# Kernel tuning notes

Hardware: AMD Instinct MI355X
Metric: run time of the kernel (lower is better)

## Reference

```python
import jax, jax.numpy as jnp
import numpy as np

B, L, H, M, E, NH, R = 4, 512, 1024, 128, 64, 16, 1024   # docs, seq, hidden, mentions, entities, heads, pairs
D, BLK, C = 768, 64, 97                                   # embed_size, block_size, num_class


def setup_inputs() -> dict:
    key = jax.random.key(0)
    ks = jax.random.split(key, 9)
    seq_lhs = jax.random.normal(ks[0], (B, L, H), jnp.float32)
    ent_lhs = jax.random.normal(ks[1], (B, M, H), jnp.float32)
    ent_to_seq_attn = jax.random.uniform(ks[2], (B, NH, M, L), jnp.float32)
    entity_id_labels = jax.random.randint(ks[3], (B, M), 0, E, jnp.int32)
    hts = jax.random.randint(ks[4], (B, R, 2), 0, E, jnp.int32)
    Wh = jax.random.normal(ks[5], (2 * H, D), jnp.float32) * 0.02
    Wt = jax.random.normal(ks[6], (2 * H, D), jnp.float32) * 0.02
    Wb = jax.random.normal(ks[7], (D * BLK, C), jnp.float32) * 0.02
    return dict(seq_lhs=seq_lhs, ent_lhs=ent_lhs, ent_to_seq_attn=ent_to_seq_attn,
                entity_id_labels=entity_id_labels, hts=hts,
                Wh=Wh, bh=jnp.zeros((D,), jnp.float32),
                Wt=Wt, bt=jnp.zeros((D,), jnp.float32),
                Wb=Wb, bb=jnp.zeros((C,), jnp.float32))


def reference(seq_lhs, ent_lhs, ent_to_seq_attn, entity_id_labels, hts, Wh, bh, Wt, bt, Wb, bb):
    # --- hrt_pool: segment logsumexp / mean over mentions per entity ---
    mask = entity_id_labels[:, None, :] == jnp.arange(E, dtype=entity_id_labels.dtype)[None, :, None]  # [B,E,M]
    cnt = mask.sum(-1)  # [B,E]
    neg = jnp.asarray(-1e30, ent_lhs.dtype)
    masked = jnp.where(mask[..., None], ent_lhs[:, None, :, :], neg)          # [B,E,M,H]
    lse = jax.nn.logsumexp(masked, axis=2)                                    # [B,E,H]
    ent_emb = jnp.where((cnt > 0)[..., None], lse, 0.0)
    mf = mask.astype(ent_to_seq_attn.dtype)
    attn_sum = jnp.einsum('bem,bhml->behl', mf, ent_to_seq_attn)              # [B,E,NH,L]
    denom = jnp.maximum(cnt, 1).astype(attn_sum.dtype)[..., None, None]
    ent_attn = jnp.where((cnt > 0)[..., None, None], attn_sum / denom, 0.0)
    # --- gather head/tail entities per pair ---
    h_idx, t_idx = hts[..., 0], hts[..., 1]                                   # [B,R]
    hs = jnp.take_along_axis(ent_emb, h_idx[..., None], axis=1)               # [B,R,H]
    ts = jnp.take_along_axis(ent_emb, t_idx[..., None], axis=1)
    h_attn = jnp.take_along_axis(ent_attn, h_idx[..., None, None], axis=1)    # [B,R,NH,L]
    t_attn = jnp.take_along_axis(ent_attn, t_idx[..., None, None], axis=1)
    ht_attn = (h_attn * t_attn).mean(axis=2)                                  # [B,R,L]
    ht_attn = ht_attn / (ht_attn.sum(-1, keepdims=True) + 1e-5)
    rel = jnp.einsum('brl,bld->brd', ht_attn, seq_lhs)                        # [B,R,H]
    # --- extractors + block bilinear ---
    hcat = jnp.concatenate([hs, rel], -1).reshape(B * R, 2 * H)
    tcat = jnp.concatenate([ts, rel], -1).reshape(B * R, 2 * H)
    hv = jnp.tanh(hcat @ Wh + bh)
    tv = jnp.tanh(tcat @ Wt + bt)
    b1 = hv.reshape(-1, D // BLK, BLK)
    b2 = tv.reshape(-1, D // BLK, BLK)
    bl = (b1[:, :, :, None] * b2[:, :, None, :]).reshape(-1, D * BLK)
    return bl @ Wb + bb                                                       # [B*R, C]
```

## Files before the change

kernel.cpp:

```cpp
#include <hip/hip_runtime.h>
#include <hip/hip_bf16.h>
#include <math.h>

#define B_  4
#define L_  512
#define H_  1024
#define M_  128
#define E_  64
#define NH_ 16
#define R_  1024
#define D_  768
#define BLK_ 64
#define C_  97
#define NROW (B_*R_)
#define KB_  (D_/BLK_)

typedef __attribute__((ext_vector_type(8))) unsigned short ushort8;
typedef __attribute__((ext_vector_type(4))) unsigned short ushort4v;
typedef __attribute__((ext_vector_type(8))) short s8;
typedef __attribute__((ext_vector_type(4))) float f4;

__device__ __forceinline__ unsigned short f2bf(float x) {
    unsigned u = __builtin_bit_cast(unsigned, x);
    unsigned r = (u + 0x7fffu + ((u >> 16) & 1u)) >> 16;
    return (unsigned short)r;
}
__device__ __forceinline__ float bf2f(unsigned short h) {
    unsigned u = ((unsigned)h) << 16;
    return __builtin_bit_cast(float, u);
}
__device__ __forceinline__ float lo16f(unsigned u) { return __builtin_bit_cast(float, u << 16); }
__device__ __forceinline__ float hi16f(unsigned u) { return __builtin_bit_cast(float, u & 0xffff0000u); }

__device__ __forceinline__ void gload_lds16(const unsigned short* g, unsigned short* l)
{
    __builtin_amdgcn_global_load_lds(
        (const __attribute__((address_space(1))) unsigned int*)g,
        (__attribute__((address_space(3))) unsigned int*)l, 16, 0, 0);
}


__global__ __launch_bounds__(256) void fused_prep(
    const float* __restrict__ Wh, const float* __restrict__ Wt,
    unsigned short* __restrict__ WhT, unsigned short* __restrict__ WtT,
    const float* __restrict__ Wb, unsigned short* __restrict__ WbT,
    const float* __restrict__ seq_lhs, unsigned short* __restrict__ seqB,
    const float* __restrict__ ent_lhs, const int* __restrict__ labels,
    unsigned short* __restrict__ ent_embB,
    const float* __restrict__ attn, unsigned short* __restrict__ ent_attnB,
    const float* __restrict__ bb, const float* __restrict__ bh,
    const float* __restrict__ bt,
    float* __restrict__ out, float* __restrict__ Ph, float* __restrict__ Pt)
{
    __shared__ __attribute__((aligned(16))) float smem[6208];
    int bx = blockIdx.x, tid = threadIdx.x;

    if (bx < 3072) {
        int z = bx / 1536, rem = bx % 1536;
        int ky = rem / 24, kx = rem % 24;
        const float* in = z ? Wt : Wh;
        unsigned short* outp = z ? WtT : WhT;
        int n0 = kx*32, k0 = ky*32;
        float (*tile)[33] = (float(*)[33])smem;
        int tx = tid & 31, ty = tid >> 5;
        #pragma unroll
        for (int p = 0; p < 4; ++p)
            tile[ty + p*8][tx] = in[((size_t)(k0 + ty + p*8))*D_ + n0 + tx];
        __syncthreads();
        #pragma unroll
        for (int p = 0; p < 4; ++p) {
            int n = n0 + ty + p*8;
            outp[(size_t)n*2048 + k0 + tx] = f2bf(tile[tx][ty + p*8]);
        }
    } else if (bx < 3840) {
        int blk = bx - 3072;
        float* sW = smem;
        const float* src = Wb + (size_t)blk*64*97;
        for (int e = tid; e < 64*97; e += 256) sW[e] = src[e];
        __syncthreads();
        unsigned short* dst = WbT + (size_t)blk*128*64;
        for (int e = tid; e < 128*64; e += 256) {
            int wcq = e >> 12;
            int ct  = (e >> 10) & 3;
            int j2  = (e >> 9) & 1;
            int qd  = (e >> 7) & 3;
            int lm  = (e >> 3) & 15;
            int t   = e & 7;
            int c   = wcq*64 + ct*16 + lm;
            int j   = j2*32 + qd*8 + t;
            dst[e] = (c < C_) ? f2bf(sW[j*97 + c]) : (unsigned short)0;
        }
    } else if (bx < 4864) {
        size_t i = ((size_t)(bx - 3840)*256 + tid) * 8;
        float4 a = *(const float4*)(seq_lhs + i);
        float4 b = *(const float4*)(seq_lhs + i + 4);
        ushort8 o = { f2bf(a.x), f2bf(a.y), f2bf(a.z), f2bf(a.w),
                      f2bf(b.x), f2bf(b.y), f2bf(b.z), f2bf(b.w) };
        *(ushort8*)(seqB + i) = o;
    } else if (bx < 5120) {
        int be = bx - 4864, b = be >> 6, e = be & 63;
        int* midx = (int*)smem;
        int* scnt = (int*)smem + M_;
        if (tid == 0) *scnt = 0;
        __syncthreads();
        if (tid < M_) {
            if (labels[b*M_ + tid] == e) {
                int p = atomicAdd(scnt, 1);
                midx[p] = tid;
            }
        }
        __syncthreads();
        int cnt = *scnt;
        for (int h = tid; h < H_; h += 256) {
            float r = 0.f;
            if (cnt > 0) {
                const float* base = ent_lhs + (size_t)b*M_*H_ + h;
                float mx = -INFINITY;
                for (int k = 0; k < cnt; ++k) mx = fmaxf(mx, base[(size_t)midx[k]*H_]);
                float s = 0.f;
                for (int k = 0; k < cnt; ++k) s += expf(base[(size_t)midx[k]*H_] - mx);
                r = mx + logf(s);
            }
            ent_embB[(size_t)be*H_ + h] = f2bf(r);
        }
    } else if (bx < 9216) {
        int id = bx - 5120;
        int e = id & 63, y = id >> 6;
        int b = y >> 4, nh = y & 15;
        int* midx = (int*)smem;
        int* scnt = (int*)smem + M_;
        if (tid == 0) *scnt = 0;
        __syncthreads();
        if (tid < M_) {
            if (labels[b*M_ + tid] == e) {
                int p = atomicAdd(scnt, 1);
                midx[p] = tid;
            }
        }
        __syncthreads();
        int cnt = *scnt;
        float inv = (cnt > 0) ? 1.f/(float)cnt : 0.f;
        const float* base = attn + ((size_t)(b*NH_ + nh)*M_)*L_;
        #pragma unroll
        for (int q = 0; q < 2; ++q) {
            int l = tid + q*256;
            float s = 0.f;
            for (int k = 0; k < cnt; ++k) s += base[(size_t)midx[k]*L_ + l];
            ent_attnB[((size_t)(b*E_ + e)*NH_ + nh)*L_ + l] = f2bf(s * inv);
        }
    } else {
        int i = (bx - 9216)*256 + tid;
        if (i < NROW*C_) out[i] = bb[i % C_];
        if (i < 256*D_) {
            Ph[i] = bh[i % D_];
            Pt[i] = bt[i % D_];
        }
    }
}

__device__ __forceinline__ void gemm128_core(const unsigned short* __restrict__ A, int lda,
                                             const unsigned short* __restrict__ Bt, int ldb,
                                             int K, int row0, int col0,
                                             f4 (&acc)[4][4])
{
    __shared__ __attribute__((aligned(16))) unsigned short As[128][32];
    __shared__ __attribute__((aligned(16))) unsigned short Bs[128][32];
    int tid = threadIdx.x;
    int wave = tid >> 6, lane = tid & 63;
    int wr = wave & 1, wc = wave >> 1;
    int lm = lane & 15, quad = lane >> 4;

    for (int k0 = 0; k0 < K; k0 += 32) {
        #pragma unroll
        for (int s = 0; s < 2; ++s) {
            int ch = tid + s*256;
            int row = ch >> 2, part = ch & 3;
            gload_lds16(A  + (size_t)(row0 + row)*lda + k0 + part*8, &As[0][0] + ch*8);
            gload_lds16(Bt + (size_t)(col0 + row)*ldb + k0 + part*8, &Bs[0][0] + ch*8);
        }
        __syncthreads();
        s8 a[4], b[4];
        #pragma unroll
        for (int ti = 0; ti < 4; ++ti) a[ti] = *(const s8*)&As[wr*64 + ti*16 + lm][quad*8];
        #pragma unroll
        for (int tj = 0; tj < 4; ++tj) b[tj] = *(const s8*)&Bs[wc*64 + tj*16 + lm][quad*8];
        #pragma unroll
        for (int ti = 0; ti < 4; ++ti)
            #pragma unroll
            for (int tj = 0; tj < 4; ++tj)
                acc[ti][tj] = __builtin_amdgcn_mfma_f32_16x16x32_bf16(a[ti], b[tj], acc[ti][tj], 0, 0, 0);
        __syncthreads();
    }
}

__global__ __launch_bounds__(256) void fused_mid(
    const unsigned short* __restrict__ ent_embB,
    const unsigned short* __restrict__ WhT, const unsigned short* __restrict__ WtT,
    float* __restrict__ Ph, float* __restrict__ Pt,
    const unsigned short* __restrict__ seqB, unsigned short* __restrict__ SWT,
    const unsigned short* __restrict__ entA, const int* __restrict__ hts,
    unsigned short* __restrict__ htA)
{
    int bx = blockIdx.x;
    if (bx < 96) {
        int x = bx % 6, y = (bx / 6) % 8, z = bx / 48;
        const unsigned short* Bt = z ? WtT : WhT;
        float* P = z ? Pt : Ph;
        int mt = y & 1, ks = y >> 1;
        int row0 = mt*128, col0 = x*128;
        f4 acc[4][4] = {};
        gemm128_core(ent_embB + ks*256, H_, Bt + ks*256, 2048, 256, row0, col0, acc);
        int lane = threadIdx.x & 63, wave = threadIdx.x >> 6;
        int wr = wave & 1, wc = wave >> 1, lm = lane & 15, quad = lane >> 4;
        #pragma unroll
        for (int ti = 0; ti < 4; ++ti)
            #pragma unroll
            for (int tj = 0; tj < 4; ++tj)
                #pragma unroll
                for (int r = 0; r < 4; ++r) {
                    int row = row0 + wr*64 + ti*16 + quad*4 + r;
                    int col = col0 + wc*64 + tj*16 + lm;
                    atomicAdd(P + (size_t)row*D_ + col, acc[ti][tj][r]);
                }
    } else if (bx < 288) {
        int id = bx - 96;
        int x = id % 4, y = (id / 4) % 6, bz = id / 24;
        int z = bz >> 2, b = bz & 3;
        const unsigned short* A  = (z ? WtT : WhT) + 1024;
        const unsigned short* Bt = seqB + (size_t)b*L_*H_;
        int row0 = y*128, col0 = x*128;
        f4 acc[4][4] = {};
        gemm128_core(A, 2048, Bt, H_, H_, row0, col0, acc);
        unsigned short* Cb = SWT + ((size_t)(z*B_ + b)*D_)*L_;
        int lane = threadIdx.x & 63, wave = threadIdx.x >> 6;
        int wr = wave & 1, wc = wave >> 1, lm = lane & 15, quad = lane >> 4;
        #pragma unroll
        for (int ti = 0; ti < 4; ++ti)
            #pragma unroll
            for (int tj = 0; tj < 4; ++tj)
                #pragma unroll
                for (int r = 0; r < 4; ++r) {
                    int d = row0 + wr*64 + ti*16 + quad*4 + r;
                    int l = col0 + wc*64 + tj*16 + lm;
                    Cb[(size_t)d*L_ + l] = f2bf(acc[ti][tj][r]);
                }
    } else {
        int id = bx - 288;
        int w  = threadIdx.x >> 6, ln = threadIdx.x & 63;
        int br = id*4 + w, b = br >> 10;
        int hi = hts[br*2 + 0], ti = hts[br*2 + 1];
        const unsigned* ph = (const unsigned*)(entA + ((size_t)(b*E_ + hi)*NH_)*L_);
        const unsigned* pt = (const unsigned*)(entA + ((size_t)(b*E_ + ti)*NH_)*L_);
        float v0[4] = {0.f, 0.f, 0.f, 0.f};
        float v1[4] = {0.f, 0.f, 0.f, 0.f};
        #pragma unroll
        for (int nh = 0; nh < NH_; ++nh) {
            #pragma unroll
            for (int c = 0; c < 4; ++c) {
                int l2 = ln + c*64;
                unsigned a = ph[nh*(L_/2) + l2], d = pt[nh*(L_/2) + l2];
                v0[c] += lo16f(a)*lo16f(d);
                v1[c] += hi16f(a)*hi16f(d);
            }
        }
        float part = 0.f;
        #pragma unroll
        for (int c = 0; c < 4; ++c) part += v0[c] + v1[c];
        #pragma unroll
        for (int off = 32; off > 0; off >>= 1) part += __shfl_xor(part, off, 64);
        float norm = 1.f / (part*(1.f/16.f) + 1e-5f);
        #pragma unroll
        for (int c = 0; c < 4; ++c) {
            unsigned short o0 = f2bf(v0[c]*(1.f/16.f)*norm);
            unsigned short o1 = f2bf(v1[c]*(1.f/16.f)*norm);
            *(unsigned*)(htA + (size_t)br*L_ + (size_t)(ln + c*64)*2) = ((unsigned)o1 << 16) | o0;
        }
    }
}

__global__ __launch_bounds__(256) void gemm_ext_mfma(
    const unsigned short* __restrict__ htA,
    const unsigned short* __restrict__ SWT,
    const float* __restrict__ Ph, const float* __restrict__ Pt,
    const int* __restrict__ hts,
    unsigned short* __restrict__ hvB, unsigned short* __restrict__ tvB)
{
    int z = blockIdx.z;
    const float* P = z ? Pt : Ph;
    unsigned short* Cv = z ? tvB : hvB;
    int row0 = blockIdx.y*128, col0 = blockIdx.x*128;
    int b = row0 >> 10;
    const unsigned short* Bt = SWT + ((size_t)(z*B_ + b)*D_)*L_;
    f4 acc[4][4] = {};
    gemm128_core(htA, L_, Bt, L_, L_, row0, col0, acc);
    int lane = threadIdx.x & 63, wave = threadIdx.x >> 6;
    int wr = wave & 1, wc = wave >> 1, lm = lane & 15, quad = lane >> 4;
    #pragma unroll
    for (int ti = 0; ti < 4; ++ti)
        #pragma unroll
        for (int r = 0; r < 4; ++r) {
            int row = row0 + wr*64 + ti*16 + quad*4 + r;
            int idx = hts[row*2 + z];
            const float* prow = P + ((size_t)(b*E_ + idx))*D_;
            #pragma unroll
            for (int tj = 0; tj < 4; ++tj) {
                int col = col0 + wc*64 + tj*16 + lm;
                float x = acc[ti][tj][r] + prow[col];
                float e = __expf(2.f*x);
                Cv[(size_t)row*D_ + col] = f2bf(1.f - 2.f/(e + 1.f));
            }
        }
}

__device__ __forceinline__ void loadB_frag(const unsigned short* __restrict__ bbase,
                                           int i, s8 (&dst)[4][2])
{
    #pragma unroll
    for (int ct = 0; ct < 4; ++ct) {
        dst[ct][0] = *(const s8*)(bbase + (size_t)i*8192 + ct*1024);
        dst[ct][1] = *(const s8*)(bbase + (size_t)i*8192 + ct*1024 + 512);
    }
}

__device__ __forceinline__ void compute_i4(const s8 (&bfr)[4][2],
                                           const float (&sh)[4],
                                           const float (&tvv)[4][2][8],
                                           f4 (&acc)[4][4])
{
    s8 afr[4][2];
    #pragma unroll
    for (int rt = 0; rt < 4; ++rt)
        #pragma unroll
        for (int j2 = 0; j2 < 2; ++j2) {
            union { unsigned u[4]; s8 v; } cv;
            #pragma unroll
            for (int t2 = 0; t2 < 4; ++t2) {
                float pe = sh[rt] * tvv[rt][j2][t2*2];
                float po = sh[rt] * tvv[rt][j2][t2*2 + 1];
                cv.u[t2] = __builtin_amdgcn_perm(__builtin_bit_cast(unsigned, po),
                                                 __builtin_bit_cast(unsigned, pe),
                                                 0x07060302u);
            }
            afr[rt][j2] = cv.v;
        }
    #pragma unroll
    for (int ct = 0; ct < 4; ++ct)
        #pragma unroll
        for (int rt = 0; rt < 4; ++rt) {
            acc[rt][ct] = __builtin_amdgcn_mfma_f32_16x16x32_bf16(afr[rt][0], bfr[ct][0], acc[rt][ct], 0, 0, 0);
            acc[rt][ct] = __builtin_amdgcn_mfma_f32_16x16x32_bf16(afr[rt][1], bfr[ct][1], acc[rt][ct], 0, 0, 0);
        }
}

__global__ __launch_bounds__(256) void final_mfma(
    const unsigned short* __restrict__ hvB,
    const unsigned short* __restrict__ tvB,
    const unsigned short* __restrict__ WbT,
    float* __restrict__ out)
{
    int kb   = blockIdx.x;
    int row0 = blockIdx.y * 128;
    __shared__ __attribute__((aligned(16))) unsigned short hS[128][72];
    __shared__ __attribute__((aligned(16))) unsigned short tS[128][72];

    int tid = threadIdx.x;
    for (int e = tid; e < 1024; e += 256) {
        int r = e >> 3, part = e & 7;
        *(ushort8*)&hS[r][part*8] = *(const ushort8*)(hvB + (size_t)(row0 + r)*D_ + kb*BLK_ + part*8);
        *(ushort8*)&tS[r][part*8] = *(const ushort8*)(tvB + (size_t)(row0 + r)*D_ + kb*BLK_ + part*8);
    }
    int wave = tid >> 6, lane = tid & 63;
    int wr = wave & 1, wc = wave >> 1;
    int lm = lane & 15, quad = lane >> 4;
    __syncthreads();

    float tvv[4][2][8];
    #pragma unroll
    for (int rt = 0; rt < 4; ++rt)
        #pragma unroll
        for (int j2 = 0; j2 < 2; ++j2) {
            int r = wr*64 + rt*16 + lm;
            ushort8 w = *(const ushort8*)&tS[r][j2*32 + quad*8];
            #pragma unroll
            for (int t = 0; t < 8; ++t) tvv[rt][j2][t] = bf2f(w[t]);
        }

    f4 acc[4][4] = {};
    const unsigned short* bbase = WbT + (size_t)kb*(64*128*64)
                                + (size_t)wc*4096 + ((size_t)quad*16 + lm)*8;

    s8 bufA[4][2], bufB[4][2];
    loadB_frag(bbase, 0, bufA);
    for (int i0 = 0; i0 < 64; i0 += 2) {
        loadB_frag(bbase, i0 + 1, bufB);
        {
            float sh[4];
            #pragma unroll
            for (int rt = 0; rt < 4; ++rt) sh[rt] = bf2f(hS[wr*64 + rt*16 + lm][i0]);
            compute_i4(bufA, sh, tvv, acc);
        }
        if (i0 < 62) loadB_frag(bbase, i0 + 2, bufA);
        {
            float sh[4];
            #pragma unroll
            for (int rt = 0; rt < 4; ++rt) sh[rt] = bf2f(hS[wr*64 + rt*16 + lm][i0 + 1]);
            compute_i4(bufB, sh, tvv, acc);
        }
    }

    #pragma unroll
    for (int rt = 0; rt < 4; ++rt)
        #pragma unroll
        for (int ct = 0; ct < 4; ++ct)
            #pragma unroll
            for (int r = 0; r < 4; ++r) {
                int row = row0 + wr*64 + rt*16 + quad*4 + r;
                int col = wc*64 + ct*16 + lm;
                if (col < C_) atomicAdd(out + (size_t)row*C_ + col, acc[rt][ct][r]);
            }
}

extern "C" void kernel_launch(void* const* d_in, const int* in_sizes, int n_in,
                              void* d_out, int out_size, void* d_ws, size_t ws_size,
                              hipStream_t stream)
{
    const float* seq_lhs = (const float*)d_in[0];
    const float* ent_lhs = (const float*)d_in[1];
    const float* attn    = (const float*)d_in[2];
    const int*   labels  = (const int*)d_in[3];
    const int*   hts     = (const int*)d_in[4];
    const float* Wh      = (const float*)d_in[5];
    const float* bh      = (const float*)d_in[6];
    const float* Wt      = (const float*)d_in[7];
    const float* bt      = (const float*)d_in[8];
    const float* Wb      = (const float*)d_in[9];
    const float* bb      = (const float*)d_in[10];
    float* out = (float*)d_out;

    float* wsf      = (float*)d_ws;
    float* Ph       = wsf;
    float* Pt       = Ph + 196608;
    unsigned short* hvB       = (unsigned short*)(Pt + 196608);
    unsigned short* tvB       = hvB       + 3145728;
    unsigned short* ent_embB  = tvB       + 3145728;
    unsigned short* ent_attnB = ent_embB  + 262144;
    unsigned short* htA       = ent_attnB + 2097152;
    unsigned short* seqB      = htA       + 2097152;
    unsigned short* WhT       = seqB      + 2097152;
    unsigned short* WtT       = WhT       + 1572864;
    unsigned short* SWT       = WtT       + 1572864;
    unsigned short* WbT       = SWT       + 3145728;

    fused_prep<<<10768, 256, 0, stream>>>(Wh, Wt, WhT, WtT, Wb, WbT,
                                          seq_lhs, seqB, ent_lhs, labels, ent_embB,
                                          attn, ent_attnB, bb, bh, bt, out, Ph, Pt);
    fused_mid<<<1312, 256, 0, stream>>>(ent_embB, WhT, WtT, Ph, Pt,
                                        seqB, SWT, ent_attnB, hts, htA);
    gemm_ext_mfma<<<dim3(6, 32, 2), 256, 0, stream>>>(htA, SWT, Ph, Pt, hts, hvB, tvB);
    final_mfma<<<dim3(KB_, NROW/128), 256, 0, stream>>>(hvB, tvB, WbT, out);
}
```

Before: 244.5 us.

## Stage Wb tiles through double-buffered LDS with direct global-to-LDS loads

The final bilinear MFMA kernel no longer loads Wb fragments straight from global memory into registers. Each 8192-element Wb slice is now copied cooperatively into a double-buffered LDS array with gload_lds16, and the next slice is prefetched while the current one feeds the MFMAs. The aim is coalesced, asynchronous weight traffic and fewer live registers. In exchange it adds 32KB of LDS per block, which may cut occupancy, and a __syncthreads on every one of the 64 iterations.

```diff
diff --git a/kernel.cpp b/kernel.cpp
--- a/kernel.cpp
+++ b/kernel.cpp
@@ -312,46 +312,6 @@
         }
 }
 
-__device__ __forceinline__ void loadB_frag(const unsigned short* __restrict__ bbase,
-                                           int i, s8 (&dst)[4][2])
-{
-    #pragma unroll
-    for (int ct = 0; ct < 4; ++ct) {
-        dst[ct][0] = *(const s8*)(bbase + (size_t)i*8192 + ct*1024);
-        dst[ct][1] = *(const s8*)(bbase + (size_t)i*8192 + ct*1024 + 512);
-    }
-}
-
-__device__ __forceinline__ void compute_i4(const s8 (&bfr)[4][2],
-                                           const float (&sh)[4],
-                                           const float (&tvv)[4][2][8],
-                                           f4 (&acc)[4][4])
-{
-    s8 afr[4][2];
-    #pragma unroll
-    for (int rt = 0; rt < 4; ++rt)
-        #pragma unroll
-        for (int j2 = 0; j2 < 2; ++j2) {
-            union { unsigned u[4]; s8 v; } cv;
-            #pragma unroll
-            for (int t2 = 0; t2 < 4; ++t2) {
-                float pe = sh[rt] * tvv[rt][j2][t2*2];
-                float po = sh[rt] * tvv[rt][j2][t2*2 + 1];
-                cv.u[t2] = __builtin_amdgcn_perm(__builtin_bit_cast(unsigned, po),
-                                                 __builtin_bit_cast(unsigned, pe),
-                                                 0x07060302u);
-            }
-            afr[rt][j2] = cv.v;
-        }
-    #pragma unroll
-    for (int ct = 0; ct < 4; ++ct)
-        #pragma unroll
-        for (int rt = 0; rt < 4; ++rt) {
-            acc[rt][ct] = __builtin_amdgcn_mfma_f32_16x16x32_bf16(afr[rt][0], bfr[ct][0], acc[rt][ct], 0, 0, 0);
-            acc[rt][ct] = __builtin_amdgcn_mfma_f32_16x16x32_bf16(afr[rt][1], bfr[ct][1], acc[rt][ct], 0, 0, 0);
-        }
-}
-
 __global__ __launch_bounds__(256) void final_mfma(
     const unsigned short* __restrict__ hvB,
     const unsigned short* __restrict__ tvB,
@@ -362,6 +322,7 @@
     int row0 = blockIdx.y * 128;
     __shared__ __attribute__((aligned(16))) unsigned short hS[128][72];
     __shared__ __attribute__((aligned(16))) unsigned short tS[128][72];
+    __shared__ __attribute__((aligned(16))) unsigned short Bs[2][8192];
 
     int tid = threadIdx.x;
     for (int e = tid; e < 1024; e += 256) {
@@ -372,6 +333,11 @@
     int wave = tid >> 6, lane = tid & 63;
     int wr = wave & 1, wc = wave >> 1;
     int lm = lane & 15, quad = lane >> 4;
+
+    const unsigned short* wbase = WbT + (size_t)kb*(64*128*64);
+    #pragma unroll
+    for (int s = 0; s < 4; ++s)
+        gload_lds16(wbase + (size_t)(tid + s*256)*8, &Bs[0][0] + (tid + s*256)*8);
     __syncthreads();
 
     float tvv[4][2][8];
@@ -386,26 +352,46 @@
         }
 
     f4 acc[4][4] = {};
-    const unsigned short* bbase = WbT + (size_t)kb*(64*128*64)
-                                + (size_t)wc*4096 + ((size_t)quad*16 + lm)*8;
-
-    s8 bufA[4][2], bufB[4][2];
-    loadB_frag(bbase, 0, bufA);
-    for (int i0 = 0; i0 < 64; i0 += 2) {
-        loadB_frag(bbase, i0 + 1, bufB);
-        {
-            float sh[4];
-            #pragma unroll
-            for (int rt = 0; rt < 4; ++rt) sh[rt] = bf2f(hS[wr*64 + rt*16 + lm][i0]);
-            compute_i4(bufA, sh, tvv, acc);
-        }
-        if (i0 < 62) loadB_frag(bbase, i0 + 2, bufA);
-        {
-            float sh[4];
-            #pragma unroll
-            for (int rt = 0; rt < 4; ++rt) sh[rt] = bf2f(hS[wr*64 + rt*16 + lm][i0 + 1]);
-            compute_i4(bufB, sh, tvv, acc);
-        }
+    int fb = wc*4096 + (quad*16 + lm)*8;
+
+    for (int i = 0; i < 64; ++i) {
+        int cur = i & 1;
+        if (i < 63) {
+            const unsigned short* g = wbase + (size_t)(i + 1)*8192;
+            #pragma unroll
+            for (int s = 0; s < 4; ++s)
+                gload_lds16(g + (size_t)(tid + s*256)*8, &Bs[cur ^ 1][0] + (tid + s*256)*8);
+        }
+        float sh[4];
+        #pragma unroll
+        for (int rt = 0; rt < 4; ++rt) sh[rt] = bf2f(hS[wr*64 + rt*16 + lm][i]);
+        s8 afr[4][2];
+        #pragma unroll
+        for (int rt = 0; rt < 4; ++rt)
+            #pragma unroll
+            for (int j2 = 0; j2 < 2; ++j2) {
+                union { unsigned u[4]; s8 v; } cv;
+                #pragma unroll
+                for (int t2 = 0; t2 < 4; ++t2) {
+                    float pe = sh[rt] * tvv[rt][j2][t2*2];
+                    float po = sh[rt] * tvv[rt][j2][t2*2 + 1];
+                    cv.u[t2] = __builtin_amdgcn_perm(__builtin_bit_cast(unsigned, po),
+                                                     __builtin_bit_cast(unsigned, pe),
+                                                     0x07060302u);
+                }
+                afr[rt][j2] = cv.v;
+            }
+        #pragma unroll
+        for (int ct = 0; ct < 4; ++ct) {
+            s8 b0 = *(const s8*)&Bs[cur][fb + ct*1024];
+            s8 b1 = *(const s8*)&Bs[cur][fb + ct*1024 + 512];
+            #pragma unroll
+            for (int rt = 0; rt < 4; ++rt) {
+                acc[rt][ct] = __builtin_amdgcn_mfma_f32_16x16x32_bf16(afr[rt][0], b0, acc[rt][ct], 0, 0, 0);
+                acc[rt][ct] = __builtin_amdgcn_mfma_f32_16x16x32_bf16(afr[rt][1], b1, acc[rt][ct], 0, 0, 0);
+            }
+        }
+        __syncthreads();
     }
 
     #pragma unroll
```

After: 255.2 us. 4.4% more time.
